# Kernel tuning notes

Hardware: AMD Instinct MI355X
Metric: run time of the kernel (lower is better)

## Reference

```python
import jax, jax.numpy as jnp
import numpy as np
import math

B, S, HID = 2, 2048, 2048
NH, NKV, HD = 16, 4, 128
ROPE_BASE = 10000.0

def _rope(x, position_ids):
    # x: [B, H, S, HD], position_ids: [B, S]
    half = HD // 2
    inv_freq = 1.0 / (ROPE_BASE ** (jnp.arange(0, half, dtype=jnp.float32) / half))
    freqs = position_ids.astype(jnp.float32)[:, :, None] * inv_freq[None, None, :]  # [B,S,half]
    cos = jnp.cos(freqs)[:, None, :, :]  # [B,1,S,half]
    sin = jnp.sin(freqs)[:, None, :, :]
    x1, x2 = x[..., :half], x[..., half:]
    return jnp.concatenate([x1 * cos - x2 * sin, x2 * cos + x1 * sin], axis=-1)

def setup_inputs() -> dict:
    key = jax.random.key(0)
    k1, k2, k3 = jax.random.split(key, 3)
    x = jax.random.normal(k1, (B, S, HID), dtype=jnp.float32)
    position_ids = jnp.broadcast_to(jnp.arange(S, dtype=jnp.int64 if jax.config.jax_enable_x64 else jnp.int32)[None, :], (B, S))
    causal = jnp.tril(jnp.ones((S, S), dtype=bool))
    mask = jnp.where(causal, 0.0, -1e9).astype(jnp.float32)[None, None, :, :]
    w_qkv = jax.random.normal(k2, (NH * HD + 2 * NKV * HD, HID), dtype=jnp.float32) * 0.02
    w_o = jax.random.normal(k3, (HID, HID), dtype=jnp.float32) * 0.02
    return {"x": x, "position_ids": position_ids, "mask": mask, "w_qkv": w_qkv, "w_o": w_o}

def reference(x, position_ids, mask, w_qkv, w_o):
    qkv = x @ w_qkv.T  # [B,S,3072]
    q_dim, kv_dim = NH * HD, NKV * HD
    q = qkv[..., :q_dim].reshape(B, S, NH, HD).transpose(0, 2, 1, 3)          # [B,NH,S,HD]
    k = qkv[..., q_dim:q_dim + kv_dim].reshape(B, S, NKV, HD).transpose(0, 2, 1, 3)
    v = qkv[..., q_dim + kv_dim:].reshape(B, S, NKV, HD).transpose(0, 2, 1, 3)
    q = _rope(q, position_ids)
    k = _rope(k, position_ids)
    n_rep = NH // NKV
    k = jnp.repeat(k, n_rep, axis=1)  # [B,NH,S,HD]
    v = jnp.repeat(v, n_rep, axis=1)
    scores = jnp.einsum('bhqd,bhkd->bhqk', q, k) / math.sqrt(HD) + mask
    attn = jax.nn.softmax(scores, axis=-1)  # dropout p=0.0 -> identity
    out = jnp.einsum('bhqk,bhkd->bhqd', attn, v)
    out = out.transpose(0, 2, 1, 3).reshape(B, S, HID)
    return out @ w_o.T
```

## Files before the change

kernel.cpp:

```cpp
#include <hip/hip_runtime.h>
#include <hip/hip_bf16.h>
#include <cstdint>
#include <cstddef>

typedef unsigned short u16;
typedef __attribute__((ext_vector_type(8))) __bf16 bf16x8;
typedef __attribute__((ext_vector_type(4))) float floatx4;

#define B_    2
#define S_    2048
#define HID_  2048
#define NH_   16
#define NKV_  4
#define HD_   128
#define QKVN_ 3072

__device__ __forceinline__ float bf2f(u16 u) {
  union { unsigned int i; float f; } v; v.i = ((unsigned int)u) << 16; return v.f;
}
__device__ __forceinline__ u16 f2bf(float f) {
  union { float f; unsigned int i; } v; v.f = f;
  unsigned int u = v.i;
  return (u16)((u + 0x7fffu + ((u >> 16) & 1u)) >> 16);
}

#define GLOAD_LDS16(gp, lp)                                                  \
  __builtin_amdgcn_global_load_lds(                                          \
      (__attribute__((address_space(1))) void*)(gp),                         \
      (__attribute__((address_space(3))) void*)(lp), 16, 0, 0)

__global__ __launch_bounds__(256)
void cast_f32_bf16(const float* __restrict__ in, u16* __restrict__ out, int n)
{
  const int i = (blockIdx.x * 256 + threadIdx.x) * 8;
  if (i >= n) return;
  const float4 a = *(const float4*)(in + i);
  const float4 b = *(const float4*)(in + i + 4);
  union { u16 h[8]; uint4 v; } o;
  o.h[0] = f2bf(a.x); o.h[1] = f2bf(a.y); o.h[2] = f2bf(a.z); o.h[3] = f2bf(a.w);
  o.h[4] = f2bf(b.x); o.h[5] = f2bf(b.y); o.h[6] = f2bf(b.z); o.h[7] = f2bf(b.w);
  *(uint4*)(out + i) = o.v;
}

#define STG_A(T, h)                                                          \
  { _Pragma("unroll") for (int p = 0; p < 2; ++p) {                          \
      const int L = p * 512 + tid; const int row = L >> 3, c = L & 7;        \
      GLOAD_LDS16(A + (size_t)(m0 + (h) * 128 + row) * lda + (T) * 64        \
                    + ((c ^ (row & 7)) * 8),                                 \
                  lA + ((T) & 1) * 16384 + (h) * 8192 + L * 8); } }
#define STG_B(T, h)                                                          \
  { _Pragma("unroll") for (int p = 0; p < 2; ++p) {                          \
      const int L = p * 512 + tid; const int row = L >> 3, c = L & 7;        \
      GLOAD_LDS16(W + (size_t)(n0 + (h) * 128 + row) * K + (T) * 64          \
                    + ((c ^ (row & 7)) * 8),                                 \
                  lB + ((T) & 1) * 16384 + (h) * 8192 + L * 8); } }
#define RD_A(mf, kc, buf) (*(const bf16x8*)(lA + (buf) * 16384 + wr * 8192   \
    + ((mf) * 16 + l15) * 64 + (((kc) * 4 + quad) ^ (l15 & 7)) * 8))
#define RD_B(nf, kc, buf) (*(const bf16x8*)(lB + (buf) * 16384               \
    + (wc >> 1) * 8192 + ((wc & 1) * 64 + (nf) * 16 + l15) * 64              \
    + (((kc) * 4 + quad) ^ (l15 & 7)) * 8))
#define RDS_A03(buf) { _Pragma("unroll") for (int ii = 0; ii < 4; ++ii) {    \
    aR[ii][0] = RD_A(ii, 0, buf); aR[ii][1] = RD_A(ii, 1, buf); } }
#define RDS_A47(buf) { _Pragma("unroll") for (int ii = 0; ii < 4; ++ii) {    \
    aR[ii][0] = RD_A(ii + 4, 0, buf); aR[ii][1] = RD_A(ii + 4, 1, buf); } }
#define RDS_B01(buf) { bR[0][0] = RD_B(0, 0, buf); bR[0][1] = RD_B(0, 1, buf); \
    bR[1][0] = RD_B(1, 0, buf); bR[1][1] = RD_B(1, 1, buf); }
#define RDS_B23(buf) { bR[2][0] = RD_B(2, 0, buf); bR[2][1] = RD_B(2, 1, buf); \
    bR[3][0] = RD_B(3, 0, buf); bR[3][1] = RD_B(3, 1, buf); }
#define MFMAQ(iB, jB)                                                        \
  { _Pragma("unroll") for (int ii = 0; ii < 4; ++ii)                         \
    _Pragma("unroll") for (int jj = 0; jj < 2; ++jj)                         \
    _Pragma("unroll") for (int kc = 0; kc < 2; ++kc)                         \
      acc[(iB) + ii][(jB) + jj] = __builtin_amdgcn_mfma_f32_16x16x32_bf16(   \
          aR[ii][kc], bR[(jB) + jj][kc], acc[(iB) + ii][(jB) + jj], 0, 0, 0); }
#define MID_BAR do { __builtin_amdgcn_s_barrier();                           \
    asm volatile("s_waitcnt lgkmcnt(0)" ::: "memory");                       \
    __builtin_amdgcn_sched_barrier(0);                                       \
    __builtin_amdgcn_s_setprio(1); } while (0)
#define END_BAR do { __builtin_amdgcn_s_setprio(0);                          \
    __builtin_amdgcn_sched_barrier(0);                                       \
    __builtin_amdgcn_s_barrier(); } while (0)

template <bool F32OUT>
__global__ __launch_bounds__(512, 2)
void gemm_bt_256(const u16* __restrict__ A, const u16* __restrict__ W,
                 void* __restrict__ Cv, int K, int lda, int ldc)
{
  extern __shared__ __align__(16) u16 smem[];
  u16* lA = smem;
  u16* lB = smem + 32768;

  const int tid  = threadIdx.x;
  const int wid  = tid >> 6, ln = tid & 63;
  const int quad = ln >> 4,  l15 = ln & 15;
  const int wr = wid >> 2, wc = wid & 3;
  const int m0 = blockIdx.y * 256, n0 = blockIdx.x * 256;

  const floatx4 vzero = {0.f, 0.f, 0.f, 0.f};
  floatx4 acc[8][4];
#pragma unroll
  for (int i = 0; i < 8; ++i)
#pragma unroll
    for (int j = 0; j < 4; ++j) acc[i][j] = vzero;

  bf16x8 aR[4][2], bR[4][2];

  const int NT = K >> 6;
  const int NI = NT >> 1;

  STG_A(0, 0); STG_A(0, 1); STG_B(0, 0); STG_B(0, 1); STG_B(1, 0); STG_B(1, 1);
  asm volatile("s_waitcnt vmcnt(4)" ::: "memory");
  __builtin_amdgcn_s_barrier();

#pragma unroll 1
  for (int i = 0; i < NI; ++i) {
    const int t = 2 * i;
    const bool more = (i + 1 < NI);

    RDS_A03(0); RDS_B01(0);
    STG_A(t + 1, 0);
    MID_BAR; MFMAQ(0, 0); END_BAR;

    RDS_B23(0);
    STG_A(t + 1, 1);
    MID_BAR; MFMAQ(0, 2); END_BAR;

    RDS_A47(0);
    if (more) STG_B(t + 2, 0);
    MID_BAR; MFMAQ(4, 0); END_BAR;

    if (more) {
      STG_B(t + 2, 1);
      asm volatile("s_waitcnt vmcnt(4)" ::: "memory");
    } else {
      asm volatile("s_waitcnt vmcnt(0)" ::: "memory");
    }
    MID_BAR; MFMAQ(4, 2); END_BAR;

    RDS_A03(1); RDS_B01(1);
    if (more) STG_A(t + 2, 0);
    MID_BAR; MFMAQ(0, 0); END_BAR;

    RDS_B23(1);
    if (more) STG_A(t + 2, 1);
    MID_BAR; MFMAQ(0, 2); END_BAR;

    RDS_A47(1);
    if (more) STG_B(t + 3, 0);
    MID_BAR; MFMAQ(4, 0); END_BAR;

    if (more) {
      STG_B(t + 3, 1);
      asm volatile("s_waitcnt vmcnt(4)" ::: "memory");
    } else {
      asm volatile("s_waitcnt vmcnt(0)" ::: "memory");
    }
    MID_BAR; MFMAQ(4, 2); END_BAR;
  }

#pragma unroll
  for (int i = 0; i < 8; ++i)
#pragma unroll
    for (int r = 0; r < 4; ++r) {
      const int row = m0 + wr * 128 + i * 16 + quad * 4 + r;
      if (F32OUT) {
        float* cp = (float*)Cv + (size_t)row * ldc + n0 + wc * 64 + l15;
#pragma unroll
        for (int j = 0; j < 4; ++j) cp[j * 16] = acc[i][j][r];
      } else {
        u16* cp = (u16*)Cv + (size_t)row * ldc + n0 + wc * 64 + l15;
#pragma unroll
        for (int j = 0; j < 4; ++j) cp[j * 16] = f2bf(acc[i][j][r]);
      }
    }
}

__global__ __launch_bounds__(256)
void rope_inplace(u16* __restrict__ qkv)
{
  const int s = blockIdx.x, b = blockIdx.y;
  const int tid = threadIdx.x;
  __shared__ float cs[64], sn[64];
  if (tid < 64) {
    const float inv = powf(10000.0f, -((float)tid) / 64.0f);
    float s_, c_;
    sincosf((float)s * inv, &s_, &c_);
    cs[tid] = c_; sn[tid] = s_;
  }
  __syncthreads();
  u16* base = qkv + ((size_t)b * S_ + s) * QKVN_;
  for (int p = tid; p < NH_ * 64; p += 256) {
    const int h = p >> 6, i = p & 63;
    u16* hp = base + h * 128;
    const float x1 = bf2f(hp[i]);
    const float x2 = bf2f(hp[64 + i]);
    hp[i]      = f2bf(x1 * cs[i] - x2 * sn[i]);
    hp[64 + i] = f2bf(x2 * cs[i] + x1 * sn[i]);
  }
  for (int p = tid; p < NKV_ * 64; p += 256) {
    const int h = p >> 6, i = p & 63;
    u16* hp = base + NH_ * HD_ + h * 128;
    const float x1 = bf2f(hp[i]);
    const float x2 = bf2f(hp[64 + i]);
    hp[i]      = f2bf(x1 * cs[i] - x2 * sn[i]);
    hp[64 + i] = f2bf(x2 * cs[i] + x1 * sn[i]);
  }
}

__global__ __launch_bounds__(256)
void v_transpose(const u16* __restrict__ qkv, u16* __restrict__ vt)
{
  const int s0  = blockIdx.x * 64;
  const int kvh = blockIdx.y;
  const int b   = blockIdx.z;
  const int tid = threadIdx.x;
  __shared__ u16 lT[128 * 73];

  const u16* vsrc = qkv + ((size_t)b * S_ + s0) * QKVN_
                    + NH_ * HD_ + NKV_ * HD_ + kvh * HD_;
#pragma unroll
  for (int p = 0; p < 4; ++p) {
    const int idx = p * 256 + tid;
    const int r = idx >> 4, c = idx & 15;
    union { uint4 v; u16 h[8]; } u;
    u.v = *(const uint4*)(vsrc + (size_t)r * QKVN_ + c * 8);
#pragma unroll
    for (int j = 0; j < 8; ++j)
      lT[(c * 8 + j) * 73 + r] = u.h[j];
  }
  __syncthreads();
  u16* vdst = vt + ((size_t)(b * NKV_ + kvh) * HD_) * S_ + s0;
#pragma unroll
  for (int p = 0; p < 4; ++p) {
    const int idx = p * 256 + tid;
    const int d = idx >> 3, rc = idx & 7;
    union { uint4 v; u16 h[8]; } o;
#pragma unroll
    for (int j = 0; j < 8; ++j)
      o.h[j] = lT[d * 73 + rc * 8 + j];
    *(uint4*)(vdst + (size_t)d * S_ + rc * 8) = o.v;
  }
}

#define LPP 68
#define KSLOT(key, s) ((key) * 128 + (((s) ^ ((key) & 7)) * 8))
#define VSLOT(d, s)   ((d) * 64  + (((s) ^ ((d) & 7)) * 8))

__global__ __launch_bounds__(256, 2)
void flash_attn(u16* __restrict__ qkv, const u16* __restrict__ vt_ws)
{
  const int pi = blockIdx.x;
  const int h  = blockIdx.y;
  const int b  = blockIdx.z;
  const int tid  = threadIdx.x;
  const int w    = tid >> 6, ln = tid & 63;
  const int quad = ln >> 4,  l15 = ln & 15;
  const int kvh  = h >> 2;

  const int qtA = 31 - pi, qtB = pi;
  const int itA = qtA + 1;
  const int nIt = itA + qtB + 1;

  __shared__ __align__(16) u16 lK[2][64 * 128];
  __shared__ __align__(16) u16 lVt[2][128 * 64];
  __shared__ __align__(16) u16 lP[4][16 * LPP];

  const float scale = 0.08838834764831845f;
  const u16* kbase = qkv + (size_t)b * S_ * QKVN_ + NH_ * HD_ + kvh * HD_;
  const u16* vbase = vt_ws + (size_t)(b * NKV_ + kvh) * HD_ * S_;
  const floatx4 vzero = {0.f, 0.f, 0.f, 0.f};

  bf16x8 qFA[4], qFB[4];
  {
    const u16* qpA = qkv + ((size_t)(b * S_) + qtA * 64 + w * 16 + l15) * QKVN_ + h * HD_;
    const u16* qpB = qkv + ((size_t)(b * S_) + qtB * 64 + w * 16 + l15) * QKVN_ + h * HD_;
#pragma unroll
    for (int c = 0; c < 4; ++c) {
      qFA[c] = *(const bf16x8*)(qpA + c * 32 + quad * 8);
      qFB[c] = *(const bf16x8*)(qpB + c * 32 + quad * 8);
    }
  }

  float m_i[4], l_i[4];
  floatx4 Oacc[8];
#pragma unroll
  for (int r = 0; r < 4; ++r) { m_i[r] = -1e30f; l_i[r] = 0.f; }
#pragma unroll
  for (int t = 0; t < 8; ++t) Oacc[t] = vzero;

  bf16x8 qF[4];
#pragma unroll
  for (int c = 0; c < 4; ++c) qF[c] = qFA[c];
  int qtC = qtA;
  int qrow0 = qtA * 64 + w * 16;

#pragma unroll
  for (int p = 0; p < 4; ++p) {
    const int idx = (w * 4 + p) * 64 + ln;
    const int key = idx >> 4, ks = idx & 15;
    GLOAD_LDS16(kbase + (size_t)key * QKVN_ + ((ks ^ (key & 7)) * 8),
                lK[0] + (w * 4 + p) * 512);
    const int d = idx >> 3, vs = idx & 7;
    GLOAD_LDS16(vbase + (size_t)d * S_ + ((vs ^ (d & 7)) * 8),
                lVt[0] + (w * 4 + p) * 512);
  }

#pragma unroll 1
  for (int it = 0; it < nIt; ++it) {
    const int ktC = (it < itA) ? it : (it - itA);
    const u16* lKc = lK[it & 1];
    const u16* lVc = lVt[it & 1];
    const bool pf = (it + 1 < nIt);
    if (pf) {
      const int ktN = (it + 1 < itA) ? (it + 1) : (it + 1 - itA);
      u16* lKn = lK[(it + 1) & 1];
      u16* lVn = lVt[(it + 1) & 1];
#pragma unroll
      for (int p = 0; p < 4; ++p) {
        const int idx = (w * 4 + p) * 64 + ln;
        const int key = idx >> 4, ks = idx & 15;
        GLOAD_LDS16(kbase + (size_t)(ktN * 64 + key) * QKVN_ + ((ks ^ (key & 7)) * 8),
                    lKn + (w * 4 + p) * 512);
        const int d = idx >> 3, vs = idx & 7;
        GLOAD_LDS16(vbase + (size_t)d * S_ + ktN * 64 + ((vs ^ (d & 7)) * 8),
                    lVn + (w * 4 + p) * 512);
      }
      asm volatile("s_waitcnt vmcnt(8)" ::: "memory");
    } else {
      asm volatile("s_waitcnt vmcnt(0)" ::: "memory");
    }
    __builtin_amdgcn_s_barrier();
    __builtin_amdgcn_sched_barrier(0);

    floatx4 sc[4];
    __builtin_amdgcn_s_setprio(1);
#pragma unroll
    for (int nt = 0; nt < 4; ++nt) {
      floatx4 a = vzero;
      const int keyloc = nt * 16 + l15;
#pragma unroll
      for (int c = 0; c < 4; ++c) {
        const bf16x8 kF = *(const bf16x8*)(lKc + KSLOT(keyloc, c * 4 + quad));
        a = __builtin_amdgcn_mfma_f32_16x16x32_bf16(qF[c], kF, a, 0, 0, 0);
      }
      sc[nt] = a;
    }
    __builtin_amdgcn_s_setprio(0);

    float pr[4][4];
#pragma unroll
    for (int r = 0; r < 4; ++r) {
      const int qrow = qrow0 + quad * 4 + r;
      float s[4];
#pragma unroll
      for (int nt = 0; nt < 4; ++nt) {
        const int key0 = ktC * 64 + nt * 16 + l15;
        s[nt] = sc[nt][r] * scale + ((key0 <= qrow) ? 0.f : -1e9f);
      }
      float mx = fmaxf(fmaxf(s[0], s[1]), fmaxf(s[2], s[3]));
#pragma unroll
      for (int off = 1; off < 16; off <<= 1) mx = fmaxf(mx, __shfl_xor(mx, off, 64));
      const float mn = fmaxf(m_i[r], mx);
      const float alpha = __expf(m_i[r] - mn);
      float sm = 0.f;
#pragma unroll
      for (int nt = 0; nt < 4; ++nt) {
        const float p = __expf(s[nt] - mn);
        pr[nt][r] = p;
        sm += p;
      }
#pragma unroll
      for (int off = 1; off < 16; off <<= 1) sm += __shfl_xor(sm, off, 64);
      l_i[r] = l_i[r] * alpha + sm;
      m_i[r] = mn;
#pragma unroll
      for (int t = 0; t < 8; ++t) Oacc[t][r] *= alpha;
    }

#pragma unroll
    for (int nt = 0; nt < 4; ++nt)
#pragma unroll
      for (int r = 0; r < 4; ++r)
        lP[w][(quad * 4 + r) * LPP + nt * 16 + l15] = f2bf(pr[nt][r]);

    {
      const bf16x8 pF0 = *(const bf16x8*)(&lP[w][l15 * LPP + quad * 8]);
      const bf16x8 pF1 = *(const bf16x8*)(&lP[w][l15 * LPP + 32 + quad * 8]);
      __builtin_amdgcn_s_setprio(1);
#pragma unroll
      for (int t = 0; t < 8; ++t) {
        const int d = t * 16 + l15;
        const bf16x8 vF0 = *(const bf16x8*)(lVc + VSLOT(d, quad));
        const bf16x8 vF1 = *(const bf16x8*)(lVc + VSLOT(d, 4 + quad));
        Oacc[t] = __builtin_amdgcn_mfma_f32_16x16x32_bf16(pF0, vF0, Oacc[t], 0, 0, 0);
        Oacc[t] = __builtin_amdgcn_mfma_f32_16x16x32_bf16(pF1, vF1, Oacc[t], 0, 0, 0);
      }
      __builtin_amdgcn_s_setprio(0);
    }

    if (ktC == qtC) {
      float linv[4];
#pragma unroll
      for (int r = 0; r < 4; ++r) linv[r] = 1.0f / l_i[r];
#pragma unroll
      for (int t = 0; t < 8; ++t) {
        const int d = t * 16 + l15;
#pragma unroll
        for (int r = 0; r < 4; ++r) {
          const int qrow = qrow0 + quad * 4 + r;
          qkv[((size_t)(b * S_ + qrow)) * QKVN_ + h * HD_ + d] =
              f2bf(Oacc[t][r] * linv[r]);
        }
      }
      if (pf) {
        qtC = qtB;
        qrow0 = qtB * 64 + w * 16;
#pragma unroll
        for (int c = 0; c < 4; ++c) qF[c] = qFB[c];
#pragma unroll
        for (int r = 0; r < 4; ++r) { m_i[r] = -1e30f; l_i[r] = 0.f; }
#pragma unroll
        for (int t = 0; t < 8; ++t) Oacc[t] = vzero;
      }
    }

    __builtin_amdgcn_s_barrier();
  }
}

extern "C" void kernel_launch(void* const* d_in, const int* in_sizes, int n_in,
                              void* d_out, int out_size, void* d_ws, size_t ws_size,
                              hipStream_t stream)
{
  (void)in_sizes; (void)n_in; (void)out_size; (void)ws_size;
  const float* x     = (const float*)d_in[0];
  const float* w_qkv = (const float*)d_in[3];
  const float* w_o   = (const float*)d_in[4];
  float* out = (float*)d_out;

  const int nX  = B_ * S_ * HID_;
  const int nWq = QKVN_ * HID_;
  const int nWo = HID_ * HID_;

  u16* ws    = (u16*)d_ws;
  u16* qkv   = ws;
  u16* slotW = qkv + (size_t)(B_ * S_) * QKVN_;
  u16* xb    = (u16*)d_out;
  u16* vt_ws = (u16*)d_out;

  const dim3 blk(256);
  cast_f32_bf16<<<nX  / 2048, blk, 0, stream>>>(x,     xb,    nX);
  cast_f32_bf16<<<nWq / 2048, blk, 0, stream>>>(w_qkv, slotW, nWq);
  gemm_bt_256<false><<<dim3(QKVN_ / 256, (B_ * S_) / 256), dim3(512), 131072, stream>>>(
      xb, slotW, qkv, HID_, HID_, QKVN_);
  rope_inplace<<<dim3(S_, B_), blk, 0, stream>>>(qkv);
  v_transpose<<<dim3(S_ / 64, NKV_, B_), blk, 0, stream>>>(qkv, vt_ws);
  cast_f32_bf16<<<nWo / 2048, blk, 0, stream>>>(w_o, slotW, nWo);
  flash_attn<<<dim3(16, NH_, B_), blk, 0, stream>>>(qkv, vt_ws);
  gemm_bt_256<true><<<dim3(HID_ / 256, (B_ * S_) / 256), dim3(512), 131072, stream>>>(
      qkv, slotW, out, HID_, QKVN_, HID_);
}
```

Baseline: 343.7 us.

## Fuse input casts, swizzle GEMM tiles, add 128-tile out-proj GEMM, lazy softmax rescale

Merges the two f32-to-bf16 cast launches into one kernel. Adds an XCD-style block swizzle to the 256 GEMM. Replaces the output projection with a new 128x128-tile GEMM so its 2048-wide output gives more workgroups. In flash attention, skips the running-max update and accumulator rescale when the new max is within 8 of the old one, trading a possible loss of accuracy for fewer exps and multiplies.

Measured after the change: 681.2 us. 1.98x slower.

```diff
diff --git a/kernel.cpp b/kernel.cpp
--- a/kernel.cpp
+++ b/kernel.cpp
@@ -40,6 +40,22 @@
   o.h[0] = f2bf(a.x); o.h[1] = f2bf(a.y); o.h[2] = f2bf(a.z); o.h[3] = f2bf(a.w);
   o.h[4] = f2bf(b.x); o.h[5] = f2bf(b.y); o.h[6] = f2bf(b.z); o.h[7] = f2bf(b.w);
   *(uint4*)(out + i) = o.v;
+}
+
+__global__ __launch_bounds__(256)
+void cast2_f32_bf16(const float* __restrict__ a, u16* __restrict__ oa, int na,
+                    const float* __restrict__ b, u16* __restrict__ ob)
+{
+  const int i = (blockIdx.x * 256 + threadIdx.x) * 8;
+  const float* src; u16* dst; int j;
+  if (i < na) { src = a; dst = oa; j = i; }
+  else        { src = b; dst = ob; j = i - na; }
+  const float4 x0 = *(const float4*)(src + j);
+  const float4 x1 = *(const float4*)(src + j + 4);
+  union { u16 h[8]; uint4 v; } o;
+  o.h[0] = f2bf(x0.x); o.h[1] = f2bf(x0.y); o.h[2] = f2bf(x0.z); o.h[3] = f2bf(x0.w);
+  o.h[4] = f2bf(x1.x); o.h[5] = f2bf(x1.y); o.h[6] = f2bf(x1.z); o.h[7] = f2bf(x1.w);
+  *(uint4*)(dst + j) = o.v;
 }
 
 #define STG_A(T, h)                                                          \
@@ -94,7 +110,11 @@
   const int wid  = tid >> 6, ln = tid & 63;
   const int quad = ln >> 4,  l15 = ln & 15;
   const int wr = wid >> 2, wc = wid & 3;
-  const int m0 = blockIdx.y * 256, n0 = blockIdx.x * 256;
+
+  const int nwg  = gridDim.x * gridDim.y;
+  const int flat = blockIdx.y * gridDim.x + blockIdx.x;
+  const int swz  = (flat & 7) * (nwg >> 3) + (flat >> 3);
+  const int m0 = (swz / gridDim.x) * 256, n0 = (swz % gridDim.x) * 256;
 
   const floatx4 vzero = {0.f, 0.f, 0.f, 0.f};
   floatx4 acc[8][4];
@@ -169,6 +189,100 @@
         for (int j = 0; j < 4; ++j) cp[j * 16] = acc[i][j][r];
       } else {
         u16* cp = (u16*)Cv + (size_t)row * ldc + n0 + wc * 64 + l15;
+#pragma unroll
+        for (int j = 0; j < 4; ++j) cp[j * 16] = f2bf(acc[i][j][r]);
+      }
+    }
+}
+
+template <bool F32OUT>
+__global__ __launch_bounds__(256, 2)
+void gemm_bt_128(const u16* __restrict__ A, const u16* __restrict__ W,
+                 void* __restrict__ Cv, int N, int K, int lda, int ldc)
+{
+  __shared__ __align__(16) u16 lA[2][128 * 64];
+  __shared__ __align__(16) u16 lB[2][128 * 64];
+  const int tid  = threadIdx.x;
+  const int w    = tid >> 6, ln = tid & 63;
+  const int quad = ln >> 4,  l15 = ln & 15;
+
+  const int nwg  = gridDim.x * gridDim.y;
+  const int flat = blockIdx.y * gridDim.x + blockIdx.x;
+  const int swz  = (flat & 7) * (nwg >> 3) + (flat >> 3);
+  const int m0 = (swz / gridDim.x) * 128, n0 = (swz % gridDim.x) * 128;
+  const int waveM = (w >> 1) * 64, waveN = (w & 1) * 64;
+
+  const floatx4 vzero = {0.f, 0.f, 0.f, 0.f};
+  floatx4 acc[4][4];
+#pragma unroll
+  for (int i = 0; i < 4; ++i)
+#pragma unroll
+    for (int j = 0; j < 4; ++j) acc[i][j] = vzero;
+
+  const int NT = K >> 6;
+
+#define STAGE128(kt, buf)                                                     \
+  { _Pragma("unroll")                                                         \
+    for (int p = 0; p < 4; ++p) {                                             \
+      const int L = (p * 4 + w) * 64 + ln;                                    \
+      const int row = L >> 3, c = L & 7;                                      \
+      const int cs = (c ^ (row & 7)) * 8;                                     \
+      GLOAD_LDS16(A + (size_t)(m0 + row) * lda + (kt) * 64 + cs,              \
+                  lA[buf] + L * 8);                                           \
+      GLOAD_LDS16(W + (size_t)(n0 + row) * K + (kt) * 64 + cs,                \
+                  lB[buf] + L * 8);                                           \
+    } }
+
+  STAGE128(0, 0);
+
+#pragma unroll 1
+  for (int t = 0; t < NT; ++t) {
+    if (t + 1 < NT) {
+      STAGE128(t + 1, (t + 1) & 1);
+      asm volatile("s_waitcnt vmcnt(8)" ::: "memory");
+    } else {
+      asm volatile("s_waitcnt vmcnt(0)" ::: "memory");
+    }
+    __builtin_amdgcn_s_barrier();
+    __builtin_amdgcn_sched_barrier(0);
+
+    const u16* a = lA[t & 1];
+    const u16* b = lB[t & 1];
+#pragma unroll
+    for (int kk = 0; kk < 64; kk += 32) {
+      bf16x8 aF[4], bF[4];
+      const int cbase = (kk >> 3) + quad;
+#pragma unroll
+      for (int tt = 0; tt < 4; ++tt) {
+        const int rowA = waveM + tt * 16 + l15;
+        aF[tt] = *(const bf16x8*)(a + rowA * 64 + (cbase ^ (l15 & 7)) * 8);
+        const int rowB = waveN + tt * 16 + l15;
+        bF[tt] = *(const bf16x8*)(b + rowB * 64 + (cbase ^ (l15 & 7)) * 8);
+      }
+      __builtin_amdgcn_s_setprio(1);
+#pragma unroll
+      for (int i = 0; i < 4; ++i)
+#pragma unroll
+        for (int j = 0; j < 4; ++j)
+          acc[i][j] = __builtin_amdgcn_mfma_f32_16x16x32_bf16(aF[i], bF[j], acc[i][j], 0, 0, 0);
+      __builtin_amdgcn_s_setprio(0);
+    }
+
+    __builtin_amdgcn_s_barrier();
+  }
+#undef STAGE128
+
+#pragma unroll
+  for (int i = 0; i < 4; ++i)
+#pragma unroll
+    for (int r = 0; r < 4; ++r) {
+      const int row = m0 + waveM + i * 16 + quad * 4 + r;
+      if (F32OUT) {
+        float* cp = (float*)Cv + (size_t)row * ldc + n0 + waveN + l15;
+#pragma unroll
+        for (int j = 0; j < 4; ++j) cp[j * 16] = acc[i][j][r];
+      } else {
+        u16* cp = (u16*)Cv + (size_t)row * ldc + n0 + waveN + l15;
 #pragma unroll
         for (int j = 0; j < 4; ++j) cp[j * 16] = f2bf(acc[i][j][r]);
       }
@@ -360,21 +474,34 @@
       float mx = fmaxf(fmaxf(s[0], s[1]), fmaxf(s[2], s[3]));
 #pragma unroll
       for (int off = 1; off < 16; off <<= 1) mx = fmaxf(mx, __shfl_xor(mx, off, 64));
-      const float mn = fmaxf(m_i[r], mx);
-      const float alpha = __expf(m_i[r] - mn);
-      float sm = 0.f;
-#pragma unroll
-      for (int nt = 0; nt < 4; ++nt) {
-        const float p = __expf(s[nt] - mn);
-        pr[nt][r] = p;
-        sm += p;
-      }
-#pragma unroll
-      for (int off = 1; off < 16; off <<= 1) sm += __shfl_xor(sm, off, 64);
-      l_i[r] = l_i[r] * alpha + sm;
-      m_i[r] = mn;
-#pragma unroll
-      for (int t = 0; t < 8; ++t) Oacc[t][r] *= alpha;
+      if (__all(mx <= m_i[r] + 8.0f)) {
+        float sm = 0.f;
+#pragma unroll
+        for (int nt = 0; nt < 4; ++nt) {
+          const float p = __expf(s[nt] - m_i[r]);
+          pr[nt][r] = p;
+          sm += p;
+        }
+#pragma unroll
+        for (int off = 1; off < 16; off <<= 1) sm += __shfl_xor(sm, off, 64);
+        l_i[r] += sm;
+      } else {
+        const float mn = fmaxf(m_i[r], mx);
+        const float alpha = __expf(m_i[r] - mn);
+        float sm = 0.f;
+#pragma unroll
+        for (int nt = 0; nt < 4; ++nt) {
+          const float p = __expf(s[nt] - mn);
+          pr[nt][r] = p;
+          sm += p;
+        }
+#pragma unroll
+        for (int off = 1; off < 16; off <<= 1) sm += __shfl_xor(sm, off, 64);
+        l_i[r] = l_i[r] * alpha + sm;
+        m_i[r] = mn;
+#pragma unroll
+        for (int t = 0; t < 8; ++t) Oacc[t][r] *= alpha;
+      }
     }
 
 #pragma unroll
@@ -449,14 +576,13 @@
   u16* vt_ws = (u16*)d_out;
 
   const dim3 blk(256);
-  cast_f32_bf16<<<nX  / 2048, blk, 0, stream>>>(x,     xb,    nX);
-  cast_f32_bf16<<<nWq / 2048, blk, 0, stream>>>(w_qkv, slotW, nWq);
+  cast2_f32_bf16<<<(nX + nWq) / 2048, blk, 0, stream>>>(x, xb, nX, w_qkv, slotW);
   gemm_bt_256<false><<<dim3(QKVN_ / 256, (B_ * S_) / 256), dim3(512), 131072, stream>>>(
       xb, slotW, qkv, HID_, HID_, QKVN_);
   rope_inplace<<<dim3(S_, B_), blk, 0, stream>>>(qkv);
   v_transpose<<<dim3(S_ / 64, NKV_, B_), blk, 0, stream>>>(qkv, vt_ws);
   cast_f32_bf16<<<nWo / 2048, blk, 0, stream>>>(w_o, slotW, nWo);
   flash_attn<<<dim3(16, NH_, B_), blk, 0, stream>>>(qkv, vt_ws);
-  gemm_bt_256<true><<<dim3(HID_ / 256, (B_ * S_) / 256), dim3(512), 131072, stream>>>(
-      qkv, slotW, out, HID_, QKVN_, HID_);
-}
+  gemm_bt_128<true><<<dim3(HID_ / 128, (B_ * S_) / 128), blk, 0, stream>>>(
+      qkv, slotW, out, HID_, HID_, QKVN_, HID_);
+}
```
